# Kernel tuning notes

Measured on AMD Instinct MI355X. Metric: run time of the kernel, lower is better.

Reference implementation:

```python
import jax, jax.numpy as jnp
import numpy as np

B, L, IN_C, OUT_C, H = 16, 4096, 256, 128, 8  # B graphs, L nodes each (static max_len)
TOTAL = B * L


def setup_inputs() -> dict:
    key = jax.random.key(0)
    k = jax.random.split(key, 7)
    x = jax.random.normal(k[0], (TOTAL, IN_C), jnp.float32)
    batch = jnp.repeat(jnp.arange(B, dtype=jnp.int32), L)  # sorted segment ids
    s = 1.0 / np.sqrt(IN_C)
    DH = OUT_C * H
    Wq = jax.random.uniform(k[1], (IN_C, DH), jnp.float32, -s, s)
    bq = jax.random.uniform(k[2], (DH,), jnp.float32, -s, s)
    Wk = jax.random.uniform(k[3], (IN_C, DH), jnp.float32, -s, s)
    bk = jax.random.uniform(k[4], (DH,), jnp.float32, -s, s)
    Wv = jax.random.uniform(k[5], (IN_C, DH), jnp.float32, -s, s)
    bv = jax.random.uniform(k[6], (DH,), jnp.float32, -s, s)
    return {"x": x, "batch": batch, "Wq": Wq, "bq": bq, "Wk": Wk, "bk": bk, "Wv": Wv, "bv": bv}


def _dense_batch_indices(batch, total):
    # position of each node within its graph (batch assumed sorted)
    counts = jax.ops.segment_sum(jnp.ones(total, jnp.int32), batch, num_segments=B)
    start = jnp.concatenate([jnp.zeros(1, jnp.int32), jnp.cumsum(counts)[:-1]])
    pos = jnp.arange(total, dtype=jnp.int32) - start[batch]
    return pos


def reference(x, batch, Wq, bq, Wk, bk, Wv, bv):
    total = x.shape[0]
    pos = _dense_batch_indices(batch, total)
    # to_dense_batch: [B, L, IN_C] with boolean mask
    xd = jnp.zeros((B, L, IN_C), x.dtype).at[batch, pos].set(x)
    mask = jnp.zeros((B, L), bool).at[batch, pos].set(True)
    m = mask[:, :, None, None]

    qs = (xd @ Wq + bq).reshape(B, L, H, OUT_C)
    ks = (xd @ Wk + bk).reshape(B, L, H, OUT_C)
    vs = (xd @ Wv + bv).reshape(B, L, H, OUT_C)
    qs = jnp.where(m, qs, 0.0)
    ks = jnp.where(m, ks, 0.0)
    vs = jnp.where(m, vs, 0.0)
    # global (Frobenius) L2 norm, matching torch.norm(t, p=2) with no dim
    qs = qs / jnp.linalg.norm(qs)
    ks = ks / jnp.linalg.norm(ks)

    N = mask.sum(axis=1).astype(x.dtype)  # nodes per graph [B]
    kvs = jnp.einsum('blhm,blhd->bhmd', ks, vs)
    attn_num = jnp.einsum('bnhm,bhmd->bnhd', qs, kvs) + N[:, None, None, None] * vs
    ks_sum = ks.sum(axis=1)  # [B,H,M]
    attn_den = jnp.einsum('bnhm,bhm->bnh', qs, ks_sum)[..., None] + N[:, None, None, None]
    attn_out = attn_num / attn_den  # [B,L,H,D]

    # gather valid nodes back to ragged layout, then mean over heads
    return attn_out[batch, pos].mean(axis=1)  # [total, OUT_C]
```

## Files before the change

kernel.cpp:

```cpp
#include <hip/hip_runtime.h>
#include <hip/hip_bf16.h>


#define TOTAL_T 65536
#define IN_C    256
#define OUT_C   128
#define NHEADS  8
#define DHID    1024

typedef __attribute__((ext_vector_type(4))) float  f32x4;
typedef __attribute__((ext_vector_type(8))) __bf16 bf16x8;

__global__ __launch_bounds__(256) void prepack_kernel(
    const float* __restrict__ Wv, const float* __restrict__ bv,
    __bf16* __restrict__ Bpack, float* __restrict__ beff)
{
    int idx = blockIdx.x * 256 + threadIdx.x;
    if (idx < 4096) {
        int lane  = idx & 63;
        int frag  = idx >> 6;
        int ntile = frag >> 3;
        int kstep = frag & 7;
        int col   = ntile * 16 + (lane & 15);
        int kbase = kstep * 32 + (lane >> 4) * 8;
        bf16x8 t;
#pragma unroll
        for (int j = 0; j < 8; ++j) {
            int k = kbase + j;
            float s = 0.f;
#pragma unroll
            for (int h = 0; h < NHEADS; ++h)
                s += Wv[(size_t)k * DHID + h * OUT_C + col];
            t[j] = (__bf16)(s * 0.125f);
        }
        *(bf16x8*)&Bpack[(size_t)idx * 8] = t;
    } else if (idx < 4096 + OUT_C) {
        int c = idx - 4096;
        float s = 0.f;
#pragma unroll
        for (int h = 0; h < NHEADS; ++h) s += bv[h * OUT_C + c];
        beff[c] = s * 0.125f;
    }
}

__global__ __launch_bounds__(256, 4) void gemm_kernel(
    const float* __restrict__ x, const __bf16* __restrict__ Bpack,
    const float* __restrict__ beff, float* __restrict__ out)
{
    const int tid  = threadIdx.x;
    const int lane = tid & 63;
    const int wid  = blockIdx.x * 4 + (tid >> 6);
    const size_t row0 = (size_t)wid * 16;
    const int lrow = lane & 15;
    const int lk   = lane >> 4;

    f32x4 acc[8];
#pragma unroll
    for (int n = 0; n < 8; ++n) acc[n] = (f32x4)0.f;

    const float* xp = x + (row0 + lrow) * IN_C + lk * 8;

    f32x4 a0 = *(const f32x4*)xp;
    f32x4 a1 = *(const f32x4*)(xp + 4);

#pragma unroll
    for (int ks = 0; ks < 8; ++ks) {
        f32x4 c0 = a0, c1 = a1;
        if (ks < 7) {
            a0 = *(const f32x4*)(xp + (ks + 1) * 32);
            a1 = *(const f32x4*)(xp + (ks + 1) * 32 + 4);
        }
        bf16x8 af;
        af[0] = (__bf16)c0[0]; af[1] = (__bf16)c0[1];
        af[2] = (__bf16)c0[2]; af[3] = (__bf16)c0[3];
        af[4] = (__bf16)c1[0]; af[5] = (__bf16)c1[1];
        af[6] = (__bf16)c1[2]; af[7] = (__bf16)c1[3];
#pragma unroll
        for (int n = 0; n < 8; ++n) {
            bf16x8 b = *(const bf16x8*)&Bpack[(size_t)((n * 8 + ks) * 64 + lane) * 8];
            acc[n] = __builtin_amdgcn_mfma_f32_16x16x32_bf16(af, b, acc[n], 0, 0, 0);
        }
    }

#pragma unroll
    for (int n = 0; n < 8; ++n) {
        float bias = beff[n * 16 + lrow];
        size_t r = row0 + lk * 4;
#pragma unroll
        for (int j = 0; j < 4; ++j)
            out[(r + j) * OUT_C + n * 16 + lrow] = acc[n][j] + bias;
    }
}

extern "C" void kernel_launch(void* const* d_in, const int* in_sizes, int n_in,
                              void* d_out, int out_size, void* d_ws, size_t ws_size,
                              hipStream_t stream)
{
    const float* x  = (const float*)d_in[0];
    const float* Wv = (const float*)d_in[6];
    const float* bv = (const float*)d_in[7];
    float* out = (float*)d_out;

    __bf16* Bpack = (__bf16*)d_ws;
    float*  beff  = (float*)((char*)d_ws + 65536);

    hipLaunchKernelGGL(prepack_kernel, dim3(17), dim3(256), 0, stream,
                       Wv, bv, Bpack, beff);
    hipLaunchKernelGGL(gemm_kernel, dim3(TOTAL_T / 64), dim3(256), 0, stream,
                       x, Bpack, beff, out);
}
```

Measured before the change: 33.09 us.

## Stage packed weight matrix in LDS and preload all x fragments up front

Each block now copies the full 64KB packed bf16 weight matrix into shared memory before computing. The MFMA loop then reads B fragments from LDS instead of global/L2. All sixteen x vector loads per lane are also issued up front to maximise memory-level parallelism. The cost is 64KB of LDS per block, a block-wide barrier, lower occupancy (launch bounds drop to 2 blocks per SM), and redundant weight copying by all 1024 blocks.

Measured after the change: 29.13 us. 1.14x faster.

```diff
diff --git a/kernel.cpp b/kernel.cpp
--- a/kernel.cpp
+++ b/kernel.cpp
@@ -43,42 +43,52 @@
     }
 }
 
-__global__ __launch_bounds__(256, 4) void gemm_kernel(
+__global__ __launch_bounds__(256, 2) void gemm_kernel(
     const float* __restrict__ x, const __bf16* __restrict__ Bpack,
     const float* __restrict__ beff, float* __restrict__ out)
 {
+    __shared__ __bf16 Blds[32768];
+
     const int tid  = threadIdx.x;
     const int lane = tid & 63;
-    const int wid  = blockIdx.x * 4 + (tid >> 6);
+    const int w    = tid >> 6;
+    const int wid  = blockIdx.x * 4 + w;
     const size_t row0 = (size_t)wid * 16;
     const int lrow = lane & 15;
     const int lk   = lane >> 4;
+
+#pragma unroll
+    for (int i = 0; i < 16; ++i) {
+        size_t off = (size_t)((w * 16 + i) * 64 + lane) * 8;
+        bf16x8 t = *(const bf16x8*)&Bpack[off];
+        *(bf16x8*)&Blds[off] = t;
+    }
+    __syncthreads();
+
+    const float* xp = x + (row0 + lrow) * IN_C + lk * 8;
+    f32x4 af32[16];
+#pragma unroll
+    for (int ks = 0; ks < 8; ++ks) {
+        af32[2 * ks]     = *(const f32x4*)(xp + ks * 32);
+        af32[2 * ks + 1] = *(const f32x4*)(xp + ks * 32 + 4);
+    }
 
     f32x4 acc[8];
 #pragma unroll
     for (int n = 0; n < 8; ++n) acc[n] = (f32x4)0.f;
 
-    const float* xp = x + (row0 + lrow) * IN_C + lk * 8;
-
-    f32x4 a0 = *(const f32x4*)xp;
-    f32x4 a1 = *(const f32x4*)(xp + 4);
-
 #pragma unroll
     for (int ks = 0; ks < 8; ++ks) {
-        f32x4 c0 = a0, c1 = a1;
-        if (ks < 7) {
-            a0 = *(const f32x4*)(xp + (ks + 1) * 32);
-            a1 = *(const f32x4*)(xp + (ks + 1) * 32 + 4);
-        }
-        bf16x8 af;
-        af[0] = (__bf16)c0[0]; af[1] = (__bf16)c0[1];
-        af[2] = (__bf16)c0[2]; af[3] = (__bf16)c0[3];
-        af[4] = (__bf16)c1[0]; af[5] = (__bf16)c1[1];
-        af[6] = (__bf16)c1[2]; af[7] = (__bf16)c1[3];
+        f32x4 v0 = af32[2 * ks], v1 = af32[2 * ks + 1];
+        bf16x8 a;
+        a[0] = (__bf16)v0[0]; a[1] = (__bf16)v0[1];
+        a[2] = (__bf16)v0[2]; a[3] = (__bf16)v0[3];
+        a[4] = (__bf16)v1[0]; a[5] = (__bf16)v1[1];
+        a[6] = (__bf16)v1[2]; a[7] = (__bf16)v1[3];
 #pragma unroll
         for (int n = 0; n < 8; ++n) {
-            bf16x8 b = *(const bf16x8*)&Bpack[(size_t)((n * 8 + ks) * 64 + lane) * 8];
-            acc[n] = __builtin_amdgcn_mfma_f32_16x16x32_bf16(af, b, acc[n], 0, 0, 0);
+            bf16x8 b = *(const bf16x8*)&Blds[(size_t)((n * 8 + ks) * 64 + lane) * 8];
+            acc[n] = __builtin_amdgcn_mfma_f32_16x16x32_bf16(a, b, acc[n], 0, 0, 0);
         }
     }
 
```
